# Kernel optimization log

Measured on AMD Instinct MI355X. Metric: run time of the kernel, lower is better.

The kernel has to match this reference:

```python
import jax, jax.numpy as jnp
import numpy as np

B, T, C = 4, 2048, 1024
N_HEAD = 16
HEAD = C // N_HEAD

def setup_inputs() -> dict:
    key = jax.random.key(0)
    k1, k2, k3 = jax.random.split(key, 3)
    x = jax.random.normal(k1, (B, T, C), dtype=jnp.float32)
    w_attn = jax.random.normal(k2, (C, 3 * C), dtype=jnp.float32) * (1.0 / np.sqrt(C))
    w_proj = jax.random.normal(k3, (C, C), dtype=jnp.float32) * (1.0 / np.sqrt(C))
    return {"x": x, "w_attn": w_attn, "w_proj": w_proj}

def reference(x, w_attn, w_proj):
    b, t, c = x.shape
    qkv = x @ w_attn  # [B,T,3C]
    q, k, v = jnp.split(qkv, 3, axis=-1)
    # [B,T,C] -> [B,H,T,D]
    def heads(z):
        return z.reshape(b, t, N_HEAD, HEAD).transpose(0, 2, 1, 3)
    q, k, v = heads(q), heads(k), heads(v)
    scale = 1.0 / np.sqrt(HEAD)
    att = jnp.einsum('bhqd,bhkd->bhqk', q, k) * scale  # [B,H,T,T]
    causal = jnp.tril(jnp.ones((t, t), dtype=bool))
    att = jnp.where(causal[None, None], att, -jnp.inf)
    att = jax.nn.softmax(att, axis=-1)
    y = jnp.einsum('bhqk,bhkd->bhqd', att, v)  # [B,H,T,D]
    y = y.transpose(0, 2, 1, 3).reshape(b, t, c)
    return y @ w_proj
```

## Files before the change

### kernel.cpp

```cpp
#include <hip/hip_runtime.h>
#include <hip/hip_bf16.h>


typedef __attribute__((ext_vector_type(8))) short bf16x8;
typedef __attribute__((ext_vector_type(4))) float f32x4;

#define T_DIM 2048
#define NHEAD 16
#define HDIM  64

__device__ __forceinline__ unsigned short f2bf(float f) {
    union { float f; unsigned int u; } v; v.f = f;
    unsigned int r = v.u + 0x7fffu + ((v.u >> 16) & 1u);
    return (unsigned short)(r >> 16);
}

__device__ __forceinline__ void gload_lds16(const void* g, void* l) {
    __builtin_amdgcn_global_load_lds(
        (const __attribute__((address_space(1))) void*)g,
        (__attribute__((address_space(3))) void*)l,
        16, 0, 0);
}

__global__ void cvt_bf16_k(const float* __restrict__ src, unsigned short* __restrict__ dst, int n) {
    int i = (blockIdx.x * blockDim.x + threadIdx.x) * 4;
    if (i < n) {
        float4 v = *(const float4*)(src + i);
        ushort4 o; o.x = f2bf(v.x); o.y = f2bf(v.y); o.z = f2bf(v.z); o.w = f2bf(v.w);
        *(ushort4*)(dst + i) = o;
    }
}

__global__ void transpose_wb_k(const float* __restrict__ src, unsigned short* __restrict__ dst,
                               int R, int Cc) {
    __shared__ float tile[32][33];
    int c0 = blockIdx.x * 32, r0 = blockIdx.y * 32;
    int tx = threadIdx.x & 31, ty = threadIdx.x >> 5;
    #pragma unroll
    for (int i = 0; i < 32; i += 8)
        tile[ty + i][tx] = src[(size_t)(r0 + ty + i) * Cc + c0 + tx];
    __syncthreads();
    #pragma unroll
    for (int i = 0; i < 32; i += 8)
        dst[(size_t)(c0 + ty + i) * R + r0 + tx] = f2bf(tile[tx][ty + i]);
}

__global__ __launch_bounds__(256) void transpose_v_k(const unsigned short* __restrict__ vb,
                                                     unsigned short* __restrict__ vt) {
    __shared__ __align__(16) unsigned short L[64 * 72];
    const int bh = blockIdx.y, t0 = blockIdx.x * 64;
    const int tid = threadIdx.x;
    const unsigned short* src = vb + ((size_t)bh * T_DIM + t0) * HDIM;
    #pragma unroll
    for (int i = 0; i < 2; ++i) {
        int cc = tid + i * 256;
        int r = cc >> 3, g = cc & 7;
        *(uint4*)&L[r * 72 + g * 8] = *(const uint4*)(src + r * 64 + g * 8);
    }
    __syncthreads();
    unsigned short* dst = vt + (size_t)bh * HDIM * T_DIM + t0;
    #pragma unroll
    for (int i = 0; i < 2; ++i) {
        int cc = tid + i * 256;
        int d = cc >> 3, gt = cc & 7;
        unsigned short tmp[8];
        #pragma unroll
        for (int j = 0; j < 8; ++j) tmp[j] = L[(gt * 8 + j) * 72 + d];
        *(uint4*)(dst + (size_t)d * T_DIM + gt * 8) = *(uint4*)tmp;
    }
}

template<int EPI>
__global__ __launch_bounds__(256) void gemm_bt_k(
    const unsigned short* __restrict__ A, const unsigned short* __restrict__ Bt,
    void* __restrict__ out0, void* __restrict__ out1, void* __restrict__ out2,
    int M, int N, int K)
{
    __shared__ __align__(16) unsigned short As[128 * 64];
    __shared__ __align__(16) unsigned short Bs[128 * 64];
    const int tid = threadIdx.x, lane = tid & 63, wave = tid >> 6;
    const int wr = wave >> 1, wc = wave & 1;

    const int nwg = gridDim.x * gridDim.y;
    const int lin = blockIdx.y * gridDim.x + blockIdx.x;
    const int lin2 = (lin & 7) * (nwg >> 3) + (lin >> 3);
    const int bxg = lin2 % gridDim.x, byg = lin2 / gridDim.x;

    const int row0 = byg * 128, col0 = bxg * 128;
    const int lrow = lane & 15, lk = (lane >> 4) * 8;

    f32x4 acc[4][4] = {};

    for (int k0 = 0; k0 < K; k0 += 64) {
        #pragma unroll
        for (int i = 0; i < 4; ++i) {
            int cb = i * 256 + wave * 64;
            int c  = cb + lane;
            gload_lds16(A  + (size_t)(row0 + (c >> 3)) * K + k0 + (c & 7) * 8, &As[cb * 8]);
            gload_lds16(Bt + (size_t)(col0 + (c >> 3)) * K + k0 + (c & 7) * 8, &Bs[cb * 8]);
        }
        __syncthreads();
        #pragma unroll
        for (int kk = 0; kk < 2; ++kk) {
            bf16x8 a[4], b[4];
            #pragma unroll
            for (int m = 0; m < 4; ++m)
                a[m] = *(const bf16x8*)&As[(wr * 64 + m * 16 + lrow) * 64 + kk * 32 + lk];
            #pragma unroll
            for (int n = 0; n < 4; ++n)
                b[n] = *(const bf16x8*)&Bs[(wc * 64 + n * 16 + lrow) * 64 + kk * 32 + lk];
            #pragma unroll
            for (int m = 0; m < 4; ++m)
                #pragma unroll
                for (int n = 0; n < 4; ++n)
                    acc[m][n] = __builtin_amdgcn_mfma_f32_16x16x32_bf16(a[m], b[n], acc[m][n], 0, 0, 0);
        }
        __syncthreads();
    }

    #pragma unroll
    for (int m = 0; m < 4; ++m) {
        #pragma unroll
        for (int n = 0; n < 4; ++n) {
            int gm0 = row0 + wr * 64 + m * 16 + (lane >> 4) * 4;
            int gn  = col0 + wc * 64 + n * 16 + (lane & 15);
            #pragma unroll
            for (int r = 0; r < 4; ++r) {
                int gm = gm0 + r;
                float v = acc[m][n][r];
                if (EPI == 0) {
                    int which = gn >> 10, rem = gn & 1023;
                    int h = rem >> 6, d = rem & 63;
                    int bb = gm >> 11, t = gm & 2047;
                    if (which == 0) v *= 0.18033688011112042f;
                    unsigned short* dst = (unsigned short*)(which == 0 ? out0 : (which == 1 ? out1 : out2));
                    dst[((size_t)(bb * NHEAD + h) * T_DIM + t) * HDIM + d] = f2bf(v);
                } else {
                    ((float*)out0)[(size_t)gm * N + gn] = v;
                }
            }
        }
    }
}

__global__ __launch_bounds__(512) void attn_k(
    const unsigned short* __restrict__ qb, const unsigned short* __restrict__ kb,
    const unsigned short* __restrict__ vtb, unsigned short* __restrict__ yb)
{
    __shared__ __align__(16) unsigned short Ks[2][64 * 64];
    __shared__ __align__(16) unsigned short Vts[2][64 * 64];
    __shared__ __align__(16) unsigned short Ps[8][16 * 72];

    const int tid = threadIdx.x, lane = tid & 63, wave = tid >> 6;
    const int bh = blockIdx.y;
    const int lrow = lane & 15, hi = lane >> 4, lk = hi * 8;
    const unsigned short* Kg  = kb  + (size_t)bh * T_DIM * HDIM;
    const unsigned short* Vtg = vtb + (size_t)bh * HDIM * T_DIM;

    const int c = wave * 64 + lane;
    const int srow = c >> 3;
    const int sgp  = (c & 7) ^ (srow & 7);
    const size_t koff = (size_t)srow * 64 + sgp * 8;
    const size_t voff = (size_t)srow * T_DIM + sgp * 8;

    bf16x8 bones;
    #pragma unroll
    for (int j = 0; j < 8; ++j) bones[j] = (lrow == 0) ? (short)0x3F80 : (short)0;

    #pragma unroll
    for (int pass = 0; pass < 2; ++pass) {
        const int bx = (pass == 0) ? (int)blockIdx.x : (15 - (int)blockIdx.x);
        const int q0 = bx * 128;
        const int jtmax = 2 * bx + 1;
        const int wrow0 = q0 + wave * 16;

        const unsigned short* qrow = qb + ((size_t)bh * T_DIM + wrow0 + lrow) * HDIM;
        bf16x8 aq0 = *(const bf16x8*)(qrow + lk);
        bf16x8 aq1 = *(const bf16x8*)(qrow + 32 + lk);

        f32x4 o[4] = {};
        f32x4 ls = {};

        gload_lds16(Kg + koff, &Ks[0][wave * 512]);
        gload_lds16(Vtg + voff, &Vts[0][wave * 512]);
        __syncthreads();

        int cur = 0;
        for (int jt = 0; jt <= jtmax; ++jt) {
            if (jt < jtmax) {
                gload_lds16(Kg + (size_t)(jt + 1) * 64 * HDIM + koff, &Ks[cur ^ 1][wave * 512]);
                gload_lds16(Vtg + (size_t)(jt + 1) * 64 + voff, &Vts[cur ^ 1][wave * 512]);
            }
            if (jt * 64 <= wrow0 + 15) {
                f32x4 s[4] = {};
                #pragma unroll
                for (int kk = 0; kk < 2; ++kk) {
                    bf16x8 aq = kk ? aq1 : aq0;
                    #pragma unroll
                    for (int n = 0; n < 4; ++n) {
                        const int row = n * 16 + lrow;
                        const int gc = (kk * 4 + hi) ^ (lrow & 7);
                        bf16x8 bk = *(const bf16x8*)&Ks[cur][row * 64 + gc * 8];
                        s[n] = __builtin_amdgcn_mfma_f32_16x16x32_bf16(aq, bk, s[n], 0, 0, 0);
                    }
                }
                const int rbase = wrow0 + hi * 4;
                if (jt * 64 + 63 > wrow0) {
                    #pragma unroll
                    for (int n = 0; n < 4; ++n) {
                        const int kvcol = jt * 64 + n * 16 + lrow;
                        #pragma unroll
                        for (int r = 0; r < 4; ++r)
                            if (kvcol > rbase + r) s[n][r] = -1e30f;
                    }
                }
                #pragma unroll
                for (int n = 0; n < 4; ++n)
                    #pragma unroll
                    for (int r = 0; r < 4; ++r) {
                        float p = __builtin_amdgcn_exp2f(s[n][r] - 16.0f);
                        Ps[wave][(hi * 4 + r) * 72 + n * 16 + lrow] = f2bf(p);
                    }
                #pragma unroll
                for (int kk = 0; kk < 2; ++kk) {
                    bf16x8 pa = *(const bf16x8*)&Ps[wave][lrow * 72 + kk * 32 + lk];
                    #pragma unroll
                    for (int dn = 0; dn < 4; ++dn) {
                        const int row = dn * 16 + lrow;
                        const int gc = (kk * 4 + hi) ^ (lrow & 7);
                        bf16x8 bv = *(const bf16x8*)&Vts[cur][row * 64 + gc * 8];
                        o[dn] = __builtin_amdgcn_mfma_f32_16x16x32_bf16(pa, bv, o[dn], 0, 0, 0);
                    }
                    ls = __builtin_amdgcn_mfma_f32_16x16x32_bf16(pa, bones, ls, 0, 0, 0);
                }
            }
            __syncthreads();
            cur ^= 1;
        }

        const int bb = bh >> 4, h = bh & 15;
        #pragma unroll
        for (int r = 0; r < 4; ++r) {
            float lsum = __shfl(ls[r], lane & 48);
            float inv = 1.0f / lsum;
            int t = q0 + wave * 16 + hi * 4 + r;
            size_t rowoff = ((size_t)(bb * T_DIM + t)) * 1024 + h * HDIM;
            #pragma unroll
            for (int dn = 0; dn < 4; ++dn)
                yb[rowoff + dn * 16 + lrow] = f2bf(o[dn][r] * inv);
        }
    }
}

extern "C" void kernel_launch(void* const* d_in, const int* in_sizes, int n_in,
                              void* d_out, int out_size, void* d_ws, size_t ws_size,
                              hipStream_t stream) {
    const float* x      = (const float*)d_in[0];
    const float* w_attn = (const float*)d_in[1];
    const float* w_proj = (const float*)d_in[2];
    float* out = (float*)d_out;

    unsigned short* xb  = (unsigned short*)d_ws;
    unsigned short* wat = xb  + (size_t)8192 * 1024;
    unsigned short* wpt = wat + (size_t)3072 * 1024;
    unsigned short* qb  = wpt + (size_t)1024 * 1024;
    unsigned short* kb  = qb  + (size_t)64 * 2048 * 64;
    unsigned short* vb  = kb  + (size_t)64 * 2048 * 64;
    unsigned short* yb  = vb  + (size_t)64 * 2048 * 64;
    unsigned short* vt  = xb;

    cvt_bf16_k<<<8192, 256, 0, stream>>>(x, xb, 8192 * 1024);
    transpose_wb_k<<<dim3(96, 32), 256, 0, stream>>>(w_attn, wat, 1024, 3072);
    transpose_wb_k<<<dim3(32, 32), 256, 0, stream>>>(w_proj, wpt, 1024, 1024);

    gemm_bt_k<0><<<dim3(24, 64), 256, 0, stream>>>(xb, wat, qb, kb, vb, 8192, 3072, 1024);
    transpose_v_k<<<dim3(32, 64), 256, 0, stream>>>(vb, vt);
    attn_k<<<dim3(8, 64), 512, 0, stream>>>(qb, kb, vt, yb);
    gemm_bt_k<1><<<dim3(8, 64), 256, 0, stream>>>(yb, wpt, out, nullptr, nullptr, 8192, 1024, 1024);
}
```

Baseline: 195.1 us.

## Rewrite bf16 GEMM with 256x256 tiles and 4-stage async LDS pipeline

```diff
diff --git a/kernel.cpp b/kernel.cpp
--- a/kernel.cpp
+++ b/kernel.cpp
@@ -71,63 +71,104 @@
 }
 
 template<int EPI>
-__global__ __launch_bounds__(256) void gemm_bt_k(
+__global__ __launch_bounds__(512, 2) void gemm_bt_k(
     const unsigned short* __restrict__ A, const unsigned short* __restrict__ Bt,
     void* __restrict__ out0, void* __restrict__ out1, void* __restrict__ out2,
     int M, int N, int K)
 {
-    __shared__ __align__(16) unsigned short As[128 * 64];
-    __shared__ __align__(16) unsigned short Bs[128 * 64];
+    extern __shared__ __align__(16) unsigned short smem[];
+    unsigned short* sA = smem;
+    unsigned short* sB = smem + 32768;
+
     const int tid = threadIdx.x, lane = tid & 63, wave = tid >> 6;
-    const int wr = wave >> 1, wc = wave & 1;
+    const int wm = wave >> 2, wn = wave & 3;
+    const int lrow = lane & 15, hi = lane >> 4;
 
     const int nwg = gridDim.x * gridDim.y;
     const int lin = blockIdx.y * gridDim.x + blockIdx.x;
     const int lin2 = (lin & 7) * (nwg >> 3) + (lin >> 3);
     const int bxg = lin2 % gridDim.x, byg = lin2 / gridDim.x;
-
-    const int row0 = byg * 128, col0 = bxg * 128;
-    const int lrow = lane & 15, lk = (lane >> 4) * 8;
-
-    f32x4 acc[4][4] = {};
-
-    for (int k0 = 0; k0 < K; k0 += 64) {
-        #pragma unroll
-        for (int i = 0; i < 4; ++i) {
-            int cb = i * 256 + wave * 64;
-            int c  = cb + lane;
-            gload_lds16(A  + (size_t)(row0 + (c >> 3)) * K + k0 + (c & 7) * 8, &As[cb * 8]);
-            gload_lds16(Bt + (size_t)(col0 + (c >> 3)) * K + k0 + (c & 7) * 8, &Bs[cb * 8]);
-        }
-        __syncthreads();
-        #pragma unroll
-        for (int kk = 0; kk < 2; ++kk) {
-            bf16x8 a[4], b[4];
+    const int row0 = byg * 256, col0 = bxg * 256;
+
+    const int ca0 = tid, ca1 = tid + 512;
+    const unsigned short* gA0 = A  + (size_t)(row0 + (ca0 & 255)) * K + (ca0 >> 8) * 8;
+    const unsigned short* gA1 = A  + (size_t)(row0 + (ca1 & 255)) * K + (ca1 >> 8) * 8;
+    const unsigned short* gB0 = Bt + (size_t)(col0 + (ca0 & 255)) * K + (ca0 >> 8) * 8;
+    const unsigned short* gB1 = Bt + (size_t)(col0 + (ca1 & 255)) * K + (ca1 >> 8) * 8;
+
+    const int NT = K >> 5;
+
+#define STAGE_A(ts) { const int sl_ = (ts) & 3; const size_t ko_ = (size_t)(ts) * 32; \
+        gload_lds16(gA0 + ko_, sA + sl_ * 8192 + ca0 * 8); \
+        gload_lds16(gA1 + ko_, sA + sl_ * 8192 + ca1 * 8); }
+#define STAGE_B(ts) { const int sl_ = (ts) & 3; const size_t ko_ = (size_t)(ts) * 32; \
+        gload_lds16(gB0 + ko_, sB + sl_ * 8192 + ca0 * 8); \
+        gload_lds16(gB1 + ko_, sB + sl_ * 8192 + ca1 * 8); }
+
+    f32x4 acc[8][4] = {};
+
+    STAGE_A(0); STAGE_B(0);
+    STAGE_A(1); STAGE_B(1);
+    STAGE_A(2); STAGE_B(2);
+    asm volatile("s_waitcnt vmcnt(8)" ::: "memory");
+    __builtin_amdgcn_s_barrier();
+
+    for (int t = 0; t < NT; ++t) {
+        const int slot = t & 3;
+        const unsigned short* As = sA + slot * 8192;
+        const unsigned short* Bs = sB + slot * 8192;
+        const int ts = t + 3;
+        const int abase = (hi * 256 + wm * 128 + lrow) * 8;
+        const int bbase = (hi * 256 + wn * 64 + lrow) * 8;
+
+        bf16x8 bfr[4], afr[4];
+        #pragma unroll
+        for (int ni = 0; ni < 4; ++ni)
+            bfr[ni] = *(const bf16x8*)&Bs[bbase + ni * 16 * 8];
+        #pragma unroll
+        for (int mi = 0; mi < 4; ++mi)
+            afr[mi] = *(const bf16x8*)&As[abase + mi * 16 * 8];
+        if (ts < NT) STAGE_A(ts);
+        __builtin_amdgcn_s_barrier();
+        __builtin_amdgcn_s_setprio(1);
+        #pragma unroll
+        for (int mi = 0; mi < 4; ++mi)
             #pragma unroll
-            for (int m = 0; m < 4; ++m)
-                a[m] = *(const bf16x8*)&As[(wr * 64 + m * 16 + lrow) * 64 + kk * 32 + lk];
+            for (int ni = 0; ni < 4; ++ni)
+                acc[mi][ni] = __builtin_amdgcn_mfma_f32_16x16x32_bf16(afr[mi], bfr[ni], acc[mi][ni], 0, 0, 0);
+        __builtin_amdgcn_s_setprio(0);
+        __builtin_amdgcn_s_barrier();
+
+        #pragma unroll
+        for (int mi = 0; mi < 4; ++mi)
+            afr[mi] = *(const bf16x8*)&As[abase + (mi + 4) * 16 * 8];
+        if (ts < NT) STAGE_B(ts);
+        __builtin_amdgcn_s_barrier();
+        __builtin_amdgcn_s_setprio(1);
+        #pragma unroll
+        for (int mi = 0; mi < 4; ++mi)
             #pragma unroll
-            for (int n = 0; n < 4; ++n)
-                b[n] = *(const bf16x8*)&Bs[(wc * 64 + n * 16 + lrow) * 64 + kk * 32 + lk];
-            #pragma unroll
-            for (int m = 0; m < 4; ++m)
-                #pragma unroll
-                for (int n = 0; n < 4; ++n)
-                    acc[m][n] = __builtin_amdgcn_mfma_f32_16x16x32_bf16(a[m], b[n], acc[m][n], 0, 0, 0);
-        }
-        __syncthreads();
-    }
-
-    #pragma unroll
-    for (int m = 0; m < 4; ++m) {
-        #pragma unroll
-        for (int n = 0; n < 4; ++n) {
-            int gm0 = row0 + wr * 64 + m * 16 + (lane >> 4) * 4;
-            int gn  = col0 + wc * 64 + n * 16 + (lane & 15);
+            for (int ni = 0; ni < 4; ++ni)
+                acc[mi + 4][ni] = __builtin_amdgcn_mfma_f32_16x16x32_bf16(afr[mi], bfr[ni], acc[mi + 4][ni], 0, 0, 0);
+        __builtin_amdgcn_s_setprio(0);
+        if (t + 3 < NT)      { asm volatile("s_waitcnt vmcnt(8)" ::: "memory"); }
+        else if (t + 2 < NT) { asm volatile("s_waitcnt vmcnt(4)" ::: "memory"); }
+        else                 { asm volatile("s_waitcnt vmcnt(0)" ::: "memory"); }
+        __builtin_amdgcn_s_barrier();
+    }
+#undef STAGE_A
+#undef STAGE_B
+
+    #pragma unroll
+    for (int mi = 0; mi < 8; ++mi) {
+        #pragma unroll
+        for (int ni = 0; ni < 4; ++ni) {
+            int gm0 = row0 + wm * 128 + mi * 16 + hi * 4;
+            int gn  = col0 + wn * 64 + ni * 16 + lrow;
             #pragma unroll
             for (int r = 0; r < 4; ++r) {
                 int gm = gm0 + r;
-                float v = acc[m][n][r];
+                float v = acc[mi][ni][r];
                 if (EPI == 0) {
                     int which = gn >> 10, rem = gn & 1023;
                     int h = rem >> 6, d = rem & 63;
@@ -269,12 +310,17 @@
     unsigned short* yb  = vb  + (size_t)64 * 2048 * 64;
     unsigned short* vt  = xb;
 
+    (void)hipFuncSetAttribute((const void*)gemm_bt_k<0>,
+                              hipFuncAttributeMaxDynamicSharedMemorySize, 131072);
+    (void)hipFuncSetAttribute((const void*)gemm_bt_k<1>,
+                              hipFuncAttributeMaxDynamicSharedMemorySize, 131072);
+
     cvt_bf16_k<<<8192, 256, 0, stream>>>(x, xb, 8192 * 1024);
     transpose_wb_k<<<dim3(96, 32), 256, 0, stream>>>(w_attn, wat, 1024, 3072);
     transpose_wb_k<<<dim3(32, 32), 256, 0, stream>>>(w_proj, wpt, 1024, 1024);
 
-    gemm_bt_k<0><<<dim3(24, 64), 256, 0, stream>>>(xb, wat, qb, kb, vb, 8192, 3072, 1024);
+    gemm_bt_k<0><<<dim3(12, 32), 512, 131072, stream>>>(xb, wat, qb, kb, vb, 8192, 3072, 1024);
     transpose_v_k<<<dim3(32, 64), 256, 0, stream>>>(vb, vt);
     attn_k<<<dim3(8, 64), 512, 0, stream>>>(qb, kb, vt, yb);
-    gemm_bt_k<1><<<dim3(8, 64), 256, 0, stream>>>(yb, wpt, out, nullptr, nullptr, 8192, 1024, 1024);
-}
+    gemm_bt_k<1><<<dim3(4, 32), 512, 131072, stream>>>(yb, wpt, out, nullptr, nullptr, 8192, 1024, 1024);
+}
```

Measured after the change: 214.0 us. 1.1x slower.

## Double-buffer GEMM LDS tiles with 256x128 blocks and k-major layout

Applied to the files above, without the earlier changes.

```diff
diff --git a/kernel.cpp b/kernel.cpp
--- a/kernel.cpp
+++ b/kernel.cpp
@@ -71,63 +71,90 @@
 }
 
 template<int EPI>
-__global__ __launch_bounds__(256) void gemm_bt_k(
+__global__ __launch_bounds__(512, 2) void gemm_bt_k(
     const unsigned short* __restrict__ A, const unsigned short* __restrict__ Bt,
     void* __restrict__ out0, void* __restrict__ out1, void* __restrict__ out2,
     int M, int N, int K)
 {
-    __shared__ __align__(16) unsigned short As[128 * 64];
-    __shared__ __align__(16) unsigned short Bs[128 * 64];
+    extern __shared__ __align__(16) unsigned short smem[];
+    unsigned short* sA = smem;
+    unsigned short* sB = smem + 32768;
+
     const int tid = threadIdx.x, lane = tid & 63, wave = tid >> 6;
-    const int wr = wave >> 1, wc = wave & 1;
+    const int wm = wave >> 1, wn = wave & 1;
+    const int lrow = lane & 15, hi = lane >> 4;
 
     const int nwg = gridDim.x * gridDim.y;
     const int lin = blockIdx.y * gridDim.x + blockIdx.x;
     const int lin2 = (lin & 7) * (nwg >> 3) + (lin >> 3);
     const int bxg = lin2 % gridDim.x, byg = lin2 / gridDim.x;
-
-    const int row0 = byg * 128, col0 = bxg * 128;
-    const int lrow = lane & 15, lk = (lane >> 4) * 8;
+    const int row0 = byg * 256, col0 = bxg * 128;
+
+    const unsigned short* gA0 = A + (size_t)(row0 + (tid & 255)) * K + (tid >> 8) * 8;
+    const unsigned short* gA1 = A + (size_t)(row0 + ((tid + 512) & 255)) * K + ((tid + 512) >> 8) * 8;
+    const unsigned short* gA2 = A + (size_t)(row0 + ((tid + 1024) & 255)) * K + ((tid + 1024) >> 8) * 8;
+    const unsigned short* gA3 = A + (size_t)(row0 + ((tid + 1536) & 255)) * K + ((tid + 1536) >> 8) * 8;
+    const unsigned short* gB0 = Bt + (size_t)(col0 + (tid & 127)) * K + (tid >> 7) * 8;
+    const unsigned short* gB1 = Bt + (size_t)(col0 + ((tid + 512) & 127)) * K + ((tid + 512) >> 7) * 8;
+
+    const int NT = K >> 6;
+
+#define STAGE(ts, bsel) { const size_t ko_ = (size_t)(ts) * 64; \
+        unsigned short* dA_ = sA + (bsel) * 16384; \
+        unsigned short* dB_ = sB + (bsel) * 8192; \
+        gload_lds16(gA0 + ko_, dA_ + tid * 8); \
+        gload_lds16(gA1 + ko_, dA_ + (tid + 512) * 8); \
+        gload_lds16(gA2 + ko_, dA_ + (tid + 1024) * 8); \
+        gload_lds16(gA3 + ko_, dA_ + (tid + 1536) * 8); \
+        gload_lds16(gB0 + ko_, dB_ + tid * 8); \
+        gload_lds16(gB1 + ko_, dB_ + (tid + 512) * 8); }
 
     f32x4 acc[4][4] = {};
 
-    for (int k0 = 0; k0 < K; k0 += 64) {
-        #pragma unroll
-        for (int i = 0; i < 4; ++i) {
-            int cb = i * 256 + wave * 64;
-            int c  = cb + lane;
-            gload_lds16(A  + (size_t)(row0 + (c >> 3)) * K + k0 + (c & 7) * 8, &As[cb * 8]);
-            gload_lds16(Bt + (size_t)(col0 + (c >> 3)) * K + k0 + (c & 7) * 8, &Bs[cb * 8]);
+    STAGE(0, 0);
+    __syncthreads();
+
+    int cur = 0;
+    for (int t = 0; t < NT; ++t) {
+        if (t + 1 < NT) STAGE(t + 1, cur ^ 1);
+
+        const unsigned short* As = sA + cur * 16384;
+        const unsigned short* Bs = sB + cur * 8192;
+        bf16x8 af[2][4], bf_[2][4];
+        #pragma unroll
+        for (int ks = 0; ks < 2; ++ks) {
+            const int kg = ks * 4 + hi;
+            #pragma unroll
+            for (int mi = 0; mi < 4; ++mi)
+                af[ks][mi] = *(const bf16x8*)&As[(kg * 256 + wm * 64 + mi * 16 + lrow) * 8];
+            #pragma unroll
+            for (int ni = 0; ni < 4; ++ni)
+                bf_[ks][ni] = *(const bf16x8*)&Bs[(kg * 128 + wn * 64 + ni * 16 + lrow) * 8];
         }
+        __builtin_amdgcn_s_setprio(1);
+        #pragma unroll
+        for (int ks = 0; ks < 2; ++ks)
+            #pragma unroll
+            for (int mi = 0; mi < 4; ++mi)
+                #pragma unroll
+                for (int ni = 0; ni < 4; ++ni)
+                    acc[mi][ni] = __builtin_amdgcn_mfma_f32_16x16x32_bf16(af[ks][mi], bf_[ks][ni], acc[mi][ni], 0, 0, 0);
+        __builtin_amdgcn_s_setprio(0);
         __syncthreads();
-        #pragma unroll
-        for (int kk = 0; kk < 2; ++kk) {
-            bf16x8 a[4], b[4];
-            #pragma unroll
-            for (int m = 0; m < 4; ++m)
-                a[m] = *(const bf16x8*)&As[(wr * 64 + m * 16 + lrow) * 64 + kk * 32 + lk];
-            #pragma unroll
-            for (int n = 0; n < 4; ++n)
-                b[n] = *(const bf16x8*)&Bs[(wc * 64 + n * 16 + lrow) * 64 + kk * 32 + lk];
-            #pragma unroll
-            for (int m = 0; m < 4; ++m)
-                #pragma unroll
-                for (int n = 0; n < 4; ++n)
-                    acc[m][n] = __builtin_amdgcn_mfma_f32_16x16x32_bf16(a[m], b[n], acc[m][n], 0, 0, 0);
-        }
-        __syncthreads();
-    }
-
-    #pragma unroll
-    for (int m = 0; m < 4; ++m) {
-        #pragma unroll
-        for (int n = 0; n < 4; ++n) {
-            int gm0 = row0 + wr * 64 + m * 16 + (lane >> 4) * 4;
-            int gn  = col0 + wc * 64 + n * 16 + (lane & 15);
+        cur ^= 1;
+    }
+#undef STAGE
+
+    #pragma unroll
+    for (int mi = 0; mi < 4; ++mi) {
+        #pragma unroll
+        for (int ni = 0; ni < 4; ++ni) {
+            int gm0 = row0 + wm * 64 + mi * 16 + hi * 4;
+            int gn  = col0 + wn * 64 + ni * 16 + lrow;
             #pragma unroll
             for (int r = 0; r < 4; ++r) {
                 int gm = gm0 + r;
-                float v = acc[m][n][r];
+                float v = acc[mi][ni][r];
                 if (EPI == 0) {
                     int which = gn >> 10, rem = gn & 1023;
                     int h = rem >> 6, d = rem & 63;
@@ -269,12 +296,17 @@
     unsigned short* yb  = vb  + (size_t)64 * 2048 * 64;
     unsigned short* vt  = xb;
 
+    (void)hipFuncSetAttribute((const void*)gemm_bt_k<0>,
+                              hipFuncAttributeMaxDynamicSharedMemorySize, 98304);
+    (void)hipFuncSetAttribute((const void*)gemm_bt_k<1>,
+                              hipFuncAttributeMaxDynamicSharedMemorySize, 98304);
+
     cvt_bf16_k<<<8192, 256, 0, stream>>>(x, xb, 8192 * 1024);
     transpose_wb_k<<<dim3(96, 32), 256, 0, stream>>>(w_attn, wat, 1024, 3072);
     transpose_wb_k<<<dim3(32, 32), 256, 0, stream>>>(w_proj, wpt, 1024, 1024);
 
-    gemm_bt_k<0><<<dim3(24, 64), 256, 0, stream>>>(xb, wat, qb, kb, vb, 8192, 3072, 1024);
+    gemm_bt_k<0><<<dim3(24, 32), 512, 98304, stream>>>(xb, wat, qb, kb, vb, 8192, 3072, 1024);
     transpose_v_k<<<dim3(32, 64), 256, 0, stream>>>(vb, vt);
     attn_k<<<dim3(8, 64), 512, 0, stream>>>(qb, kb, vt, yb);
-    gemm_bt_k<1><<<dim3(8, 64), 256, 0, stream>>>(yb, wpt, out, nullptr, nullptr, 8192, 1024, 1024);
-}
+    gemm_bt_k<1><<<dim3(8, 32), 512, 98304, stream>>>(yb, wpt, out, nullptr, nullptr, 8192, 1024, 1024);
+}
```

Result: slower. 234.8 us (+20.3%).
